# Kernel optimization log

Hardware: AMD Instinct MI355X
Metric: run time of the kernel (lower is better)

The kernel has to match this reference:

```python
import jax, jax.numpy as jnp
import numpy as np

B, D, K, E = 256, 256, 1024, 16  # batch, dim_codes, book_size, embedding_dim
DECAY = 0.999
GAIN = 1.0 - DECAY
EPS = 1e-6


def setup_inputs() -> dict:
    key = jax.random.key(0)
    k1, k2 = jax.random.split(key)
    return {
        "cw_q": jax.random.normal(k1, (B, D * E), dtype=jnp.float32),
        "codebook": jax.random.normal(k2, (D, K, E), dtype=jnp.float32),
        "ema_counts": jnp.ones((D, K), dtype=jnp.float32),
    }


def reference(cw_q, codebook, ema_counts):
    batch = cw_q.shape[0]
    x = cw_q.reshape(batch, D, E)  # [B, D, E]

    x2 = jnp.sum(x * x, axis=-1)                       # [B, D]
    c2 = jnp.sum(codebook * codebook, axis=-1)         # [D, K]
    xc = jnp.einsum('bde,dke->bdk', x, codebook)       # [B, D, K]
    dist = x2[:, :, None] + c2[None, :, :] - 2.0 * xc

    idx = jnp.argmin(dist, axis=-1)                    # [B, D] int32

    # gather nearest code vector per (batch, dim_code)
    cw_embed = codebook[jnp.arange(D)[None, :], idx]   # [B, D, E]
    cw_embed = cw_embed.reshape(batch, D * E)

    one_hot_idx = jax.nn.one_hot(idx, K, dtype=cw_q.dtype)  # [B, D, K]

    # EMA update (training path): scatter-sum of assigned vectors per code
    update = jnp.einsum('bdk,bde->dke', one_hot_idx, x)      # [D, K, E]
    new_codebook = codebook * DECAY + GAIN * update / (ema_counts[:, :, None] + EPS)
    new_ema_counts = DECAY * ema_counts + GAIN * jnp.sum(one_hot_idx, axis=0)

    return cw_embed, one_hot_idx, new_codebook, new_ema_counts
```

## Files before the change

### kernel.cpp

```cpp
#include <hip/hip_runtime.h>
#include <float.h>

#define BB 256
#define DD 256
#define KK 1024
#define EE 16
#define DECAY 0.999f
#define GAIN  0.001f
#define EPS   1e-6f

#define OH_OFF   ((size_t)BB * DD * EE)
#define CB_OFF   (OH_OFF + (size_t)BB * DD * KK)
#define EMA_OFF  (CB_OFF + (size_t)DD * KK * EE)

__device__ __forceinline__ float dot16(const float4& a0, const float4& a1,
                                       const float4& a2, const float4& a3,
                                       const float4& b0, const float4& b1,
                                       const float4& b2, const float4& b3) {
  float s = a0.x * b0.x;
  s = fmaf(a0.y, b0.y, s); s = fmaf(a0.z, b0.z, s); s = fmaf(a0.w, b0.w, s);
  s = fmaf(a1.x, b1.x, s); s = fmaf(a1.y, b1.y, s); s = fmaf(a1.z, b1.z, s); s = fmaf(a1.w, b1.w, s);
  s = fmaf(a2.x, b2.x, s); s = fmaf(a2.y, b2.y, s); s = fmaf(a2.z, b2.z, s); s = fmaf(a2.w, b2.w, s);
  s = fmaf(a3.x, b3.x, s); s = fmaf(a3.y, b3.y, s); s = fmaf(a3.z, b3.z, s); s = fmaf(a3.w, b3.w, s);
  return s;
}

__global__ __launch_bounds__(512, 2) void vqvae_fused(
    const float* __restrict__ cw_q,
    const float* __restrict__ codebook,
    const float* __restrict__ ema,
    float* __restrict__ out)
{
  __shared__ float4 cb4s[KK * EE / 4];
  __shared__ float4 upd4s[KK * EE / 4];
  __shared__ float  c2s[KK];
  __shared__ float  cnts[KK];
  __shared__ float  pbest[8 * 256];
  __shared__ int    pidxs[8 * 256];
  __shared__ int    ish[BB];

  const int t = threadIdx.x;
  const int d = blockIdx.x;
  const int w = t >> 6;
  const int l = t & 63;
  const float4 z4 = make_float4(0.f, 0.f, 0.f, 0.f);

  #pragma unroll
  for (int j = 0; j < 2; ++j) cnts[t + 512 * j] = 0.f;
  #pragma unroll
  for (int i = 0; i < 8; ++i) upd4s[i * 512 + t] = z4;

  const float4* src4 = (const float4*)codebook + (size_t)d * (KK * EE / 4);
  #pragma unroll
  for (int i = 0; i < 8; ++i) {
    int i4 = i * 512 + t;
    float4 v = src4[i4];
    cb4s[i4] = v;
    float sq = v.x * v.x;
    sq = fmaf(v.y, v.y, sq);
    sq = fmaf(v.z, v.z, sq);
    sq = fmaf(v.w, v.w, sq);
    sq += __shfl_xor(sq, 1);
    sq += __shfl_xor(sq, 2);
    if ((t & 3) == 0) c2s[i4 >> 2] = sq;
  }

  float4 xv[4][4];
  float  x2[4];
  #pragma unroll
  for (int j = 0; j < 4; ++j) {
    const int b = l + 64 * j;
    const float4* xr = (const float4*)cw_q + (size_t)b * (DD * EE / 4) + d * 4;
    xv[j][0] = xr[0]; xv[j][1] = xr[1]; xv[j][2] = xr[2]; xv[j][3] = xr[3];
  }
  __syncthreads();

  #pragma unroll
  for (int j = 0; j < 4; ++j)
    x2[j] = dot16(xv[j][0], xv[j][1], xv[j][2], xv[j][3],
                  xv[j][0], xv[j][1], xv[j][2], xv[j][3]);

  float best[4] = {FLT_MAX, FLT_MAX, FLT_MAX, FLT_MAX};
  int   bi[4]   = {0, 0, 0, 0};
  const int kbase = w << 7;

  float* ohp = out + OH_OFF;
  float4* zb = (float4*)(ohp + (size_t)(w << 5) * (DD * KK) + (size_t)d * KK) + l;

  #pragma unroll 2
  for (int s = 0; s < 128; ++s) {
    const int k = kbase + s;
    const float4* p = cb4s + (k << 2);
    float4 c0 = p[0], c1 = p[1], c2v = p[2], c3 = p[3];
    const float c2k = c2s[k];

    #pragma unroll
    for (int j = 0; j < 4; ++j) {
      float dj = dot16(c0, c1, c2v, c3, xv[j][0], xv[j][1], xv[j][2], xv[j][3]);
      float dist = fmaf(-2.f, dj, x2[j] + c2k);
      if (dist < best[j]) { best[j] = dist; bi[j] = k; }
    }

    zb[(size_t)(s >> 2) * (DD * KK / 4) + (s & 3) * 64] = z4;
  }

  #pragma unroll
  for (int j = 0; j < 4; ++j) {
    pbest[w * 256 + l + 64 * j] = best[j];
    pidxs[w * 256 + l + 64 * j] = bi[j];
  }
  __syncthreads();

  if (t < 256) {
    const int b = t;
    float bb = pbest[b];
    int   bidx = pidxs[b];
    #pragma unroll
    for (int w2 = 1; w2 < 8; ++w2) {
      float e = pbest[w2 * 256 + b];
      int   ii = pidxs[w2 * 256 + b];
      if (e < bb) { bb = e; bidx = ii; }
    }

    float4* ce = (float4*)out + (size_t)b * (DD * EE / 4) + d * 4;
    const float4* cwp = cb4s + (bidx << 2);
    ce[0] = cwp[0]; ce[1] = cwp[1]; ce[2] = cwp[2]; ce[3] = cwp[3];

    ohp[(size_t)b * (DD * KK) + (size_t)d * KK + bidx] = 1.0f;

    ish[b] = bidx;
    atomicAdd(&cnts[bidx], 1.0f);
  }
  __syncthreads();

  {
    float* upd = (float*)upd4s;
    const int e = t & 15;
    const int g = t >> 4;
    #pragma unroll
    for (int i = 0; i < 8; ++i) {
      int b = g * 8 + i;
      int k = ish[b];
      float xvv = cw_q[(size_t)b * (DD * EE) + (size_t)d * EE + e];
      atomicAdd(&upd[k * EE + e], xvv);
    }
  }
  __syncthreads();

  {
    const float* emad = ema + (size_t)d * KK;
    float* oe = out + EMA_OFF + (size_t)d * KK;
    #pragma unroll
    for (int j = 0; j < 2; ++j) {
      int k = t + 512 * j;
      float ev = emad[k];
      c2s[k] = ev;
      oe[k] = DECAY * ev + GAIN * cnts[k];
    }
  }
  __syncthreads();

  {
    float4* ocb = (float4*)(out + CB_OFF) + (size_t)d * (KK * EE / 4);
    #pragma unroll
    for (int i = 0; i < 8; ++i) {
      int i4 = i * 512 + t;
      int k  = i4 >> 2;
      float4 c = cb4s[i4];
      float4 u = upd4s[i4];
      float inv = GAIN / (c2s[k] + EPS);
      float4 r;
      r.x = DECAY * c.x + u.x * inv;
      r.y = DECAY * c.y + u.y * inv;
      r.z = DECAY * c.z + u.z * inv;
      r.w = DECAY * c.w + u.w * inv;
      ocb[i4] = r;
    }
  }
}

extern "C" void kernel_launch(void* const* d_in, const int* in_sizes, int n_in,
                              void* d_out, int out_size, void* d_ws, size_t ws_size,
                              hipStream_t stream) {
  const float* cw_q     = (const float*)d_in[0];
  const float* codebook = (const float*)d_in[1];
  const float* ema      = (const float*)d_in[2];
  float* out = (float*)d_out;
  (void)in_sizes; (void)n_in; (void)out_size; (void)d_ws; (void)ws_size;

  vqvae_fused<<<dim3(DD), dim3(512), 0, stream>>>(cw_q, codebook, ema, out);
}
```

Baseline: 318.7 us.

## Use 1024-thread blocks, atomicMin packed argmin, and nontemporal output stores

Doubles the threads per block to 1024, so each wave scans 64 codes instead of 128. The cross-wave argmin now uses a 64-bit atomicMin on packed (distance, index) keys instead of shared partial arrays and a serial reduction. All output writes become nontemporal stores, and part of the one-hot zero-fill is issued before the distance loop so it overlaps the prologue. EMA and x prefetch happen earlier, which removes a barrier. The cost is higher register pressure at 1024 threads and shared-memory atomics on the keys.

```diff
diff --git a/kernel.cpp b/kernel.cpp
--- a/kernel.cpp
+++ b/kernel.cpp
@@ -12,6 +12,8 @@
 #define OH_OFF   ((size_t)BB * DD * EE)
 #define CB_OFF   (OH_OFF + (size_t)BB * DD * KK)
 #define EMA_OFF  (CB_OFF + (size_t)DD * KK * EE)
+
+typedef float f32x4 __attribute__((ext_vector_type(4)));
 
 __device__ __forceinline__ float dot16(const float4& a0, const float4& a1,
                                        const float4& a2, const float4& a3,
@@ -25,7 +27,18 @@
   return s;
 }
 
-__global__ __launch_bounds__(512, 2) void vqvae_fused(
+__device__ __forceinline__ unsigned long long packkey(float dist, int k) {
+  unsigned u = __float_as_uint(dist);
+  unsigned m = ((int)u < 0) ? 0xFFFFFFFFu : 0x80000000u;
+  return ((unsigned long long)(u ^ m) << 32) | (unsigned long long)(unsigned)k;
+}
+
+__device__ __forceinline__ void ntst4(float4* p, float4 v) {
+  f32x4 t = { v.x, v.y, v.z, v.w };
+  __builtin_nontemporal_store(t, (f32x4*)p);
+}
+
+__global__ __launch_bounds__(1024) void vqvae_fused(
     const float* __restrict__ cw_q,
     const float* __restrict__ codebook,
     const float* __restrict__ ema,
@@ -34,9 +47,9 @@
   __shared__ float4 cb4s[KK * EE / 4];
   __shared__ float4 upd4s[KK * EE / 4];
   __shared__ float  c2s[KK];
+  __shared__ float  esh[KK];
   __shared__ float  cnts[KK];
-  __shared__ float  pbest[8 * 256];
-  __shared__ int    pidxs[8 * 256];
+  __shared__ unsigned long long amin[BB];
   __shared__ int    ish[BB];
 
   const int t = threadIdx.x;
@@ -45,15 +58,16 @@
   const int l = t & 63;
   const float4 z4 = make_float4(0.f, 0.f, 0.f, 0.f);
 
-  #pragma unroll
-  for (int j = 0; j < 2; ++j) cnts[t + 512 * j] = 0.f;
-  #pragma unroll
-  for (int i = 0; i < 8; ++i) upd4s[i * 512 + t] = z4;
+  cnts[t] = 0.f;
+  if (t < BB) amin[t] = ~0ULL;
+  esh[t] = ema[(size_t)d * KK + t];
+  #pragma unroll
+  for (int i = 0; i < 4; ++i) upd4s[i * 1024 + t] = z4;
 
   const float4* src4 = (const float4*)codebook + (size_t)d * (KK * EE / 4);
   #pragma unroll
-  for (int i = 0; i < 8; ++i) {
-    int i4 = i * 512 + t;
+  for (int i = 0; i < 4; ++i) {
+    int i4 = i * 1024 + t;
     float4 v = src4[i4];
     cb4s[i4] = v;
     float sq = v.x * v.x;
@@ -73,60 +87,71 @@
     const float4* xr = (const float4*)cw_q + (size_t)b * (DD * EE / 4) + d * 4;
     xv[j][0] = xr[0]; xv[j][1] = xr[1]; xv[j][2] = xr[2]; xv[j][3] = xr[3];
   }
-  __syncthreads();
+
+  float* ohp = out + OH_OFF;
+  float4* zb = (float4*)(ohp + (size_t)(w << 4) * (DD * KK) + (size_t)d * KK) + l;
+
+  #pragma unroll
+  for (int f = 0; f < 16; ++f)
+    ntst4(&zb[(size_t)(f >> 2) * (DD * KK / 4) + (f & 3) * 64], z4);
 
   #pragma unroll
   for (int j = 0; j < 4; ++j)
     x2[j] = dot16(xv[j][0], xv[j][1], xv[j][2], xv[j][3],
                   xv[j][0], xv[j][1], xv[j][2], xv[j][3]);
 
+  __syncthreads();
+
   float best[4] = {FLT_MAX, FLT_MAX, FLT_MAX, FLT_MAX};
   int   bi[4]   = {0, 0, 0, 0};
-  const int kbase = w << 7;
-
-  float* ohp = out + OH_OFF;
-  float4* zb = (float4*)(ohp + (size_t)(w << 5) * (DD * KK) + (size_t)d * KK) + l;
-
-  #pragma unroll 2
-  for (int s = 0; s < 128; ++s) {
+  const int kbase = w << 6;
+
+  auto body = [&](int s) {
     const int k = kbase + s;
     const float4* p = cb4s + (k << 2);
     float4 c0 = p[0], c1 = p[1], c2v = p[2], c3 = p[3];
     const float c2k = c2s[k];
-
     #pragma unroll
     for (int j = 0; j < 4; ++j) {
       float dj = dot16(c0, c1, c2v, c3, xv[j][0], xv[j][1], xv[j][2], xv[j][3]);
       float dist = fmaf(-2.f, dj, x2[j] + c2k);
       if (dist < best[j]) { best[j] = dist; bi[j] = k; }
     }
-
-    zb[(size_t)(s >> 2) * (DD * KK / 4) + (s & 3) * 64] = z4;
-  }
-
-  #pragma unroll
-  for (int j = 0; j < 4; ++j) {
-    pbest[w * 256 + l + 64 * j] = best[j];
-    pidxs[w * 256 + l + 64 * j] = bi[j];
-  }
-  __syncthreads();
-
-  if (t < 256) {
+  };
+
+  #pragma unroll 1
+  for (int s = 0; s < 48; ++s) {
+    body(s);
+    ntst4(&zb[(size_t)(4 + (s >> 2)) * (DD * KK / 4) + (s & 3) * 64], z4);
+  }
+  #pragma unroll 1
+  for (int s = 48; s < 64; ++s) body(s);
+
+  #pragma unroll
+  for (int j = 0; j < 4; ++j)
+    atomicMin(&amin[l + 64 * j], packkey(best[j], bi[j]));
+
+  __syncthreads();
+
+  const int e = t & 15;
+  const int g = t >> 4;
+  float xpre[4];
+  #pragma unroll
+  for (int i = 0; i < 4; ++i)
+    xpre[i] = cw_q[(size_t)(g * 4 + i) * (DD * EE) + (size_t)d * EE + e];
+
+  if (t < BB) {
     const int b = t;
-    float bb = pbest[b];
-    int   bidx = pidxs[b];
-    #pragma unroll
-    for (int w2 = 1; w2 < 8; ++w2) {
-      float e = pbest[w2 * 256 + b];
-      int   ii = pidxs[w2 * 256 + b];
-      if (e < bb) { bb = e; bidx = ii; }
-    }
+    unsigned long long key = amin[b];
+    const int bidx = (int)(unsigned)(key & 0xFFFFFFFFull);
 
     float4* ce = (float4*)out + (size_t)b * (DD * EE / 4) + d * 4;
     const float4* cwp = cb4s + (bidx << 2);
-    ce[0] = cwp[0]; ce[1] = cwp[1]; ce[2] = cwp[2]; ce[3] = cwp[3];
-
-    ohp[(size_t)b * (DD * KK) + (size_t)d * KK + bidx] = 1.0f;
+    ntst4(&ce[0], cwp[0]); ntst4(&ce[1], cwp[1]);
+    ntst4(&ce[2], cwp[2]); ntst4(&ce[3], cwp[3]);
+
+    __builtin_nontemporal_store(
+        1.0f, &ohp[(size_t)b * (DD * KK) + (size_t)d * KK + bidx]);
 
     ish[b] = bidx;
     atomicAdd(&cnts[bidx], 1.0f);
@@ -135,46 +160,31 @@
 
   {
     float* upd = (float*)upd4s;
-    const int e = t & 15;
-    const int g = t >> 4;
     #pragma unroll
-    for (int i = 0; i < 8; ++i) {
-      int b = g * 8 + i;
-      int k = ish[b];
-      float xvv = cw_q[(size_t)b * (DD * EE) + (size_t)d * EE + e];
-      atomicAdd(&upd[k * EE + e], xvv);
+    for (int i = 0; i < 4; ++i) {
+      int k = ish[g * 4 + i];
+      atomicAdd(&upd[k * EE + e], xpre[i]);
     }
-  }
-  __syncthreads();
-
-  {
-    const float* emad = ema + (size_t)d * KK;
     float* oe = out + EMA_OFF + (size_t)d * KK;
-    #pragma unroll
-    for (int j = 0; j < 2; ++j) {
-      int k = t + 512 * j;
-      float ev = emad[k];
-      c2s[k] = ev;
-      oe[k] = DECAY * ev + GAIN * cnts[k];
-    }
+    __builtin_nontemporal_store(DECAY * esh[t] + GAIN * cnts[t], &oe[t]);
   }
   __syncthreads();
 
   {
     float4* ocb = (float4*)(out + CB_OFF) + (size_t)d * (KK * EE / 4);
     #pragma unroll
-    for (int i = 0; i < 8; ++i) {
-      int i4 = i * 512 + t;
+    for (int i = 0; i < 4; ++i) {
+      int i4 = i * 1024 + t;
       int k  = i4 >> 2;
       float4 c = cb4s[i4];
       float4 u = upd4s[i4];
-      float inv = GAIN / (c2s[k] + EPS);
+      float inv = GAIN / (esh[k] + EPS);
       float4 r;
       r.x = DECAY * c.x + u.x * inv;
       r.y = DECAY * c.y + u.y * inv;
       r.z = DECAY * c.z + u.z * inv;
       r.w = DECAY * c.w + u.w * inv;
-      ocb[i4] = r;
+      ntst4(&ocb[i4], r);
     }
   }
 }
@@ -188,5 +198,5 @@
   float* out = (float*)d_out;
   (void)in_sizes; (void)n_in; (void)out_size; (void)d_ws; (void)ws_size;
 
-  vqvae_fused<<<dim3(DD), dim3(512), 0, stream>>>(cw_q, codebook, ema, out);
-}
+  vqvae_fused<<<dim3(DD), dim3(1024), 0, stream>>>(cw_q, codebook, ema, out);
+}
```

Measured after the change: 318.1 us. Within noise of the previous version (-0.2%).
